# Optimization experiments

Measured on AMD Instinct MI355X. Metric: run time of the kernel, lower is better.

The kernel has to match this reference:

```python
import jax, jax.numpy as jnp
import numpy as np

B, T, C = 4, 2048, 1024
NH = 16
HD = C // NH


def setup_inputs() -> dict:
    key = jax.random.key(0)
    k1, k2, k3 = jax.random.split(key, 3)
    x = jax.random.normal(k1, (B, T, C), dtype=jnp.float32)
    Wqkv = jax.random.normal(k2, (C, 3 * C), dtype=jnp.float32) * 0.02
    bqkv = jnp.zeros((3 * C,), dtype=jnp.float32)
    Wproj = jax.random.normal(k3, (C, C), dtype=jnp.float32) * 0.02
    bproj = jnp.zeros((C,), dtype=jnp.float32)
    return {"x": x, "Wqkv": Wqkv, "bqkv": bqkv, "Wproj": Wproj, "bproj": bproj}


def reference(x, Wqkv, bqkv, Wproj, bproj):
    Bx, Tx, Cx = x.shape
    qkv = x @ Wqkv + bqkv  # [B,T,3C]
    q, k, v = jnp.split(qkv, 3, axis=-1)
    # [B, NH, T, HD]
    q = q.reshape(Bx, Tx, NH, HD).transpose(0, 2, 1, 3)
    k = k.reshape(Bx, Tx, NH, HD).transpose(0, 2, 1, 3)
    v = v.reshape(Bx, Tx, NH, HD).transpose(0, 2, 1, 3)
    scale = 1.0 / jnp.sqrt(jnp.float32(HD))
    att = jnp.einsum('bhqd,bhkd->bhqk', q, k) * scale  # [B,NH,T,T]
    causal = jnp.tril(jnp.ones((Tx, Tx), dtype=bool))
    att = jnp.where(causal, att, jnp.float32(-jnp.inf))
    att = jax.nn.softmax(att, axis=-1)
    y = jnp.einsum('bhqk,bhkd->bhqd', att, v)  # [B,NH,T,HD]
    y = y.transpose(0, 2, 1, 3).reshape(Bx, Tx, Cx)
    return y @ Wproj + bproj
```

## Files before the change

### kernel.cpp

```cpp
#include <hip/hip_runtime.h>
#include <hip/hip_bf16.h>
#include <math.h>

#define B_  4
#define T_  2048
#define C_  1024
#define NH_ 16
#define HD_ 64

using bf16 = __hip_bfloat16;
typedef __attribute__((ext_vector_type(8))) short bf16x8;
typedef __attribute__((ext_vector_type(4))) short bf16x4;
typedef __attribute__((ext_vector_type(4))) float f32x4;

__device__ __forceinline__ bf16 f2b(float f){ return __float2bfloat16(f); }

__device__ __forceinline__ short f2bs(float f){
  union { float f; unsigned u; } x; x.f = f;
  x.u += 0x7FFFu + ((x.u >> 16) & 1u);
  return (short)(x.u >> 16);
}

__device__ __forceinline__ bf16x4 pack_bf16x4(float a, float b, float c, float d){
  union { bf16x4 v; __hip_bfloat162 h[2]; } u;
  u.h[0] = __float22bfloat162_rn(make_float2(a, b));
  u.h[1] = __float22bfloat162_rn(make_float2(c, d));
  return u.v;
}

__device__ __forceinline__ float fexp2(float x){
  float r; asm("v_exp_f32 %0, %1" : "=v"(r) : "v"(x)); return r;
}

__device__ __forceinline__ void async_load16(const bf16* g, bf16* l){
  __builtin_amdgcn_global_load_lds((const __attribute__((address_space(1))) unsigned int*)g,
                                   (__attribute__((address_space(3))) unsigned int*)l,
                                   16, 0, 0);
}

#define QSCALE 0.18033688011112042f

__global__ __launch_bounds__(256) void k_prep(const float* __restrict__ x, bf16* __restrict__ xb, int n,
                                              const float* __restrict__ in0, bf16* __restrict__ out0,
                                              const float* __restrict__ in1, bf16* __restrict__ out1){
  __shared__ float t[32][33];
  int b = blockIdx.x;
  if (b < 8192){
    int i = (b * 256 + threadIdx.x) * 4;
    if (i < n){
      float4 f = *(const float4*)(x + i);
      ushort4 u;
      u.x = (unsigned short)f2bs(f.x);
      u.y = (unsigned short)f2bs(f.y);
      u.z = (unsigned short)f2bs(f.z);
      u.w = (unsigned short)f2bs(f.w);
      *(ushort4*)(xb + i) = u;
    }
    return;
  }
  b -= 8192;
  const float* in; bf16* out; int Cc, bx, by;
  if (b < 3072){ in = in0; out = out0; Cc = 3*C_; bx = (b % 96)*32; by = (b / 96)*32; }
  else { b -= 3072; in = in1; out = out1; Cc = C_; bx = (b & 31)*32; by = (b >> 5)*32; }
  const int R = C_;
  int lx = threadIdx.x & 31, ly = threadIdx.x >> 5;
  #pragma unroll
  for (int s = 0; s < 4; s++){
    int k = by + ly + s*8;
    t[ly + s*8][lx] = in[(size_t)k * Cc + bx + lx];
  }
  __syncthreads();
  #pragma unroll
  for (int s = 0; s < 4; s++){
    int n2 = bx + ly + s*8;
    out[(size_t)n2 * R + by + lx] = f2b(t[lx][ly + s*8]);
  }
}

template<int MODE, int BM>
__global__ __launch_bounds__(BM*2) void k_gemm(
    const bf16* __restrict__ A, const bf16* __restrict__ BT,
    const float* __restrict__ bias,
    bf16* __restrict__ qo, bf16* __restrict__ ko, bf16* __restrict__ vo,
    float* __restrict__ fout,
    int M, int N, int K)
{
  constexpr int NTHR = BM*2;
  constexpr int WMW  = BM/64;
  constexpr int NB   = 512/NTHR;
  __shared__ bf16 As[2][BM*32];
  __shared__ bf16 Bs[2][128*32];

  const int tid  = threadIdx.x;
  const int wave = tid >> 6, lane = tid & 63;
  const int wm = wave % WMW, wn = wave / WMW;
  const int quad = lane >> 4, l15 = lane & 15;
  const int bm = blockIdx.x * BM;
  const int bn = blockIdx.y * 128;

  const bf16* gA[2]; bf16* lA[2];
  #pragma unroll
  for (int s = 0; s < 2; s++){
    const int c = tid + s*NTHR;
    const int r = c >> 2, p = (c & 3) ^ ((r >> 1) & 3);
    gA[s] = A + (size_t)(bm + r)*K + p*8;
    lA[s] = &As[0][0] + (size_t)c*8;
  }
  const bf16* gB[NB]; bf16* lB[NB];
  #pragma unroll
  for (int s = 0; s < NB; s++){
    const int c = tid + s*NTHR;
    const int r = c >> 2, p = (c & 3) ^ ((r >> 1) & 3);
    gB[s] = BT + (size_t)(bn + r)*K + p*8;
    lB[s] = &Bs[0][0] + (size_t)c*8;
  }
  const int fsw = (l15 >> 1) & 3;

  f32x4 acc[4][4] = {};
  const int nK = K >> 5;

  #pragma unroll
  for (int s = 0; s < 2; s++) async_load16(gA[s], lA[s]);
  #pragma unroll
  for (int s = 0; s < NB; s++) async_load16(gB[s], lB[s]);

  for (int kt = 0; kt < nK; kt++){
    __syncthreads();
    if (kt + 1 < nK){
      const int off = (kt + 1) * 32;
      const int ba  = ((kt + 1) & 1) * (BM*32);
      const int bb  = ((kt + 1) & 1) * 4096;
      #pragma unroll
      for (int s = 0; s < 2; s++) async_load16(gA[s] + off, lA[s] + ba);
      #pragma unroll
      for (int s = 0; s < NB; s++) async_load16(gB[s] + off, lB[s] + bb);
    }
    const bf16* as = &As[kt & 1][0];
    const bf16* bs = &Bs[kt & 1][0];

    bf16x8 af[4], bfv[4];
    #pragma unroll
    for (int i = 0; i < 4; i++)
      af[i]  = *reinterpret_cast<const bf16x8*>(as + (wm*64 + i*16 + l15)*32 + ((quad ^ fsw) << 3));
    #pragma unroll
    for (int j = 0; j < 4; j++)
      bfv[j] = *reinterpret_cast<const bf16x8*>(bs + (wn*64 + j*16 + l15)*32 + ((quad ^ fsw) << 3));
    #pragma unroll
    for (int i = 0; i < 4; i++)
      #pragma unroll
      for (int j = 0; j < 4; j++)
        acc[i][j] = __builtin_amdgcn_mfma_f32_16x16x32_bf16(af[i], bfv[j], acc[i][j], 0, 0, 0);
  }

  if (MODE == 0){
    const int sec = bn >> 10;
    const int bb2 = bm >> 11;
    const int tb  = (bm & (T_ - 1)) + wm*64 + quad*4;
    const int hn  = ((bn & 1023) >> 6) + wn;
    const size_t bhx = (size_t)(bb2 * NH_ + hn);
    if (sec == 2){
      #pragma unroll
      for (int j = 0; j < 4; j++){
        const int d = j*16 + l15;
        const float bj = bias[bn + wn*64 + j*16 + l15];
        bf16* vrow = vo + (bhx * HD_ + d) * (size_t)T_;
        const int sw = (l15 & 7) * 8;
        #pragma unroll
        for (int i = 0; i < 4; i++){
          const int t = (tb + i*16) ^ sw;
          *reinterpret_cast<bf16x4*>(vrow + t) =
            pack_bf16x4(acc[i][j][0] + bj, acc[i][j][1] + bj,
                        acc[i][j][2] + bj, acc[i][j][3] + bj);
        }
      }
    } else {
      bf16* dst = (sec == 0) ? qo : ko;
      const float sc = (sec == 0) ? QSCALE : 1.0f;
      bf16* base = dst + bhx * T_ * HD_;
      float bj[4];
      #pragma unroll
      for (int j = 0; j < 4; j++) bj[j] = bias[bn + wn*64 + j*16 + l15];
      #pragma unroll
      for (int i = 0; i < 4; i++){
        #pragma unroll
        for (int r = 0; r < 4; r++){
          const int t  = tb + i*16 + r;
          const int sw2 = (t & 7) * 8;
          bf16* prow = base + (size_t)t * HD_;
          #pragma unroll
          for (int j = 0; j < 4; j++){
            const int dq = (j*16 + l15) ^ sw2;
            short s = f2bs((acc[i][j][r] + bj[j]) * sc);
            prow[dq] = *(bf16*)&s;
          }
        }
      }
    }
  } else {
    const int n0 = bn + wn*64 + l15;
    float bj[4];
    #pragma unroll
    for (int j = 0; j < 4; j++) bj[j] = bias[n0 + j*16];
    #pragma unroll
    for (int i = 0; i < 4; i++){
      #pragma unroll
      for (int r = 0; r < 4; r++){
        float* p0 = fout + (size_t)(bm + wm*64 + i*16 + quad*4 + r) * N + n0;
        #pragma unroll
        for (int j = 0; j < 4; j++)
          p0[j*16] = acc[i][j][r] + bj[j];
      }
    }
  }
}

__global__ __launch_bounds__(256) void k_attn(
    const bf16* __restrict__ Q, const bf16* __restrict__ Kg,
    const bf16* __restrict__ Vt, bf16* __restrict__ Y)
{
  __shared__ bf16 Ks[2][64*64];
  __shared__ bf16 Vs[2][64*64];

  const int bh = blockIdx.x;
  const int bb = bh >> 4, hh = bh & 15;
  const int qt = 15 - blockIdx.y;
  const int tid  = threadIdx.x;
  const int wave = tid >> 6, lane = tid & 63;
  const int quad = lane >> 4, l15 = lane & 15;
  const int swz  = (l15 & 7) * 8;

  const size_t baseQK = (size_t)bh * T_ * HD_;
  const size_t baseV  = (size_t)bh * HD_ * T_;

  const int ca = wave, cb = wave + 4;
  const bf16* kg_a = Kg + baseQK + ca*512 + (size_t)lane*8;
  const bf16* kg_b = Kg + baseQK + cb*512 + (size_t)lane*8;
  const bf16* vg_a = Vt + baseV + (size_t)(ca*8 + (lane>>3)) * T_ + (lane&7)*8;
  const bf16* vg_b = Vt + baseV + (size_t)(cb*8 + (lane>>3)) * T_ + (lane&7)*8;
  bf16* kl_a0 = &Ks[0][0] + ca*512;  bf16* kl_b0 = &Ks[0][0] + cb*512;
  bf16* vl_a0 = &Vs[0][0] + ca*512;  bf16* vl_b0 = &Vs[0][0] + cb*512;

  bf16x4 ones_f;
  {
    short v = (l15 == 0) ? f2bs(1.0f) : (short)0;
    ones_f = (bf16x4){ v, v, v, v };
  }

  const int jmax = 2*qt + 1;

  bf16x8 qf[2][2];
  #pragma unroll
  for (int s = 0; s < 2; s++){
    const int t = qt*128 + s*64 + wave*16 + l15;
    #pragma unroll
    for (int ks = 0; ks < 2; ks++){
      const int col = (ks*32 + quad*8) ^ swz;
      qf[s][ks] = *reinterpret_cast<const bf16x8*>(Q + baseQK + (size_t)t*HD_ + col);
    }
  }

  async_load16(kg_a, kl_a0);  async_load16(kg_b, kl_b0);
  async_load16(vg_a, vl_a0);  async_load16(vg_b, vl_b0);

  f32x4 o[2][5] = {};

  for (int j = 0; j <= jmax; j++){
    __syncthreads();

    if (j < jmax){
      const int nb = ((j+1) & 1) * 4096;
      const size_t ko = (size_t)(j+1) * 64 * HD_;
      async_load16(kg_a + ko, kl_a0 + nb);  async_load16(kg_b + ko, kl_b0 + nb);
      async_load16(vg_a + (j+1)*64, vl_a0 + nb);
      async_load16(vg_b + (j+1)*64, vl_b0 + nb);
    }

    const bf16* ksb = &Ks[j & 1][0];
    const bf16* vsb = &Vs[j & 1][0];

    f32x4 st[2][4] = {};
    __builtin_amdgcn_s_setprio(1);
    #pragma unroll
    for (int ks = 0; ks < 2; ks++){
      #pragma unroll
      for (int tk = 0; tk < 4; tk++){
        bf16x8 kf = *reinterpret_cast<const bf16x8*>(ksb + (tk*16 + l15)*64 + ((ks*32 + quad*8) ^ swz));
        st[0][tk] = __builtin_amdgcn_mfma_f32_16x16x32_bf16(kf, qf[0][ks], st[0][tk], 0, 0, 0);
        st[1][tk] = __builtin_amdgcn_mfma_f32_16x16x32_bf16(kf, qf[1][ks], st[1][tk], 0, 0, 0);
      }
    }
    __builtin_amdgcn_s_setprio(0);

    bf16x4 pf[2][4];
    #pragma unroll
    for (int s = 0; s < 2; s++){
      const int qg = qt*128 + s*64 + wave*16 + l15;
      const bool msk = s ? (j > 2*qt) : (j >= 2*qt);
      #pragma unroll
      for (int tk = 0; tk < 4; tk++){
        float e[4];
        #pragma unroll
        for (int r = 0; r < 4; r++){
          float sv = st[s][tk][r];
          if (msk){
            const int kvg = j*64 + tk*16 + quad*4 + r;
            if (kvg > qg) sv = -1e30f;
          }
          e[r] = fexp2(sv);
        }
        pf[s][tk] = pack_bf16x4(e[0], e[1], e[2], e[3]);
      }
    }

    __builtin_amdgcn_s_setprio(1);
    #pragma unroll
    for (int td = 0; td < 4; td++){
      #pragma unroll
      for (int tk = 0; tk < 4; tk++){
        bf16x4 vf = *reinterpret_cast<const bf16x4*>(vsb + (td*16 + l15)*64 + ((tk*16 + quad*4) ^ swz));
        o[0][td] = __builtin_amdgcn_mfma_f32_16x16x16bf16_1k(vf, pf[0][tk], o[0][td], 0, 0, 0);
        o[1][td] = __builtin_amdgcn_mfma_f32_16x16x16bf16_1k(vf, pf[1][tk], o[1][td], 0, 0, 0);
      }
    }
    #pragma unroll
    for (int tk = 0; tk < 4; tk++){
      o[0][4] = __builtin_amdgcn_mfma_f32_16x16x16bf16_1k(ones_f, pf[0][tk], o[0][4], 0, 0, 0);
      o[1][4] = __builtin_amdgcn_mfma_f32_16x16x16bf16_1k(ones_f, pf[1][tk], o[1][4], 0, 0, 0);
    }
    __builtin_amdgcn_s_setprio(0);
  }

  #pragma unroll
  for (int s = 0; s < 2; s++){
    const float l = __shfl(o[s][4][0], l15, 64);
    const float inv = 1.0f / l;
    const int t = qt*128 + s*64 + wave*16 + l15;
    bf16* yrow = Y + ((size_t)(bb * T_ + t)) * C_ + hh * HD_;
    #pragma unroll
    for (int td = 0; td < 4; td++){
      *reinterpret_cast<bf16x4*>(yrow + td*16 + quad*4) =
        pack_bf16x4(o[s][td][0] * inv, o[s][td][1] * inv,
                    o[s][td][2] * inv, o[s][td][3] * inv);
    }
  }
}


extern "C" void kernel_launch(void* const* d_in, const int* in_sizes, int n_in,
                              void* d_out, int out_size, void* d_ws, size_t ws_size,
                              hipStream_t stream) {
  const float* x     = (const float*)d_in[0];
  const float* Wqkv  = (const float*)d_in[1];
  const float* bqkv  = (const float*)d_in[2];
  const float* Wproj = (const float*)d_in[3];
  const float* bproj = (const float*)d_in[4];
  float* out = (float*)d_out;

  const size_t M = (size_t)B_ * T_;
  char* w = (char*)d_ws;
  bf16* xb     = (bf16*)w;  w += M * C_ * 2;
  bf16* WqkvT  = (bf16*)w;  w += (size_t)3 * C_ * C_ * 2;
  bf16* WprojT = (bf16*)w;  w += (size_t)C_ * C_ * 2;
  bf16* Qb     = (bf16*)w;  w += M * C_ * 2;
  bf16* Kb     = (bf16*)w;  w += M * C_ * 2;
  bf16* Vtb    = (bf16*)w;  w += M * C_ * 2;
  bf16* Yb     = (bf16*)w;  w += M * C_ * 2;

  {
    int n = (int)(M * C_);
    k_prep<<<dim3(12288), dim3(256), 0, stream>>>(x, xb, n, Wqkv, WqkvT, Wproj, WprojT);
  }
  k_gemm<0,256><<<dim3(M/256, (3*C_)/128), dim3(512), 0, stream>>>(
      xb, WqkvT, bqkv, Qb, Kb, Vtb, nullptr, (int)M, 3*C_, C_);
  k_attn<<<dim3(64, 16), dim3(256), 0, stream>>>(Qb, Kb, Vtb, Yb);
  k_gemm<1,128><<<dim3(M/128, C_/128), dim3(256), 0, stream>>>(
      Yb, WprojT, bproj, nullptr, nullptr, nullptr, out, (int)M, C_, C_);
}
```

Before: 247.0 us.

## Rework GEMM pipeline with 64-wide K stages and manual vmcnt waits

```diff
diff --git a/kernel.cpp b/kernel.cpp
--- a/kernel.cpp
+++ b/kernel.cpp
@@ -77,79 +77,82 @@
   }
 }
 
-template<int MODE, int BM>
-__global__ __launch_bounds__(BM*2) void k_gemm(
+template<int MODE>
+__global__ __launch_bounds__(256, 2) void k_gemm8(
     const bf16* __restrict__ A, const bf16* __restrict__ BT,
     const float* __restrict__ bias,
     bf16* __restrict__ qo, bf16* __restrict__ ko, bf16* __restrict__ vo,
     float* __restrict__ fout,
     int M, int N, int K)
 {
-  constexpr int NTHR = BM*2;
-  constexpr int WMW  = BM/64;
-  constexpr int NB   = 512/NTHR;
-  __shared__ bf16 As[2][BM*32];
-  __shared__ bf16 Bs[2][128*32];
+  __shared__ bf16 As[2][2][128*32];
+  __shared__ bf16 Bs[2][2][128*32];
 
   const int tid  = threadIdx.x;
   const int wave = tid >> 6, lane = tid & 63;
-  const int wm = wave % WMW, wn = wave / WMW;
+  const int wm = wave & 1, wn = wave >> 1;
   const int quad = lane >> 4, l15 = lane & 15;
-  const int bm = blockIdx.x * BM;
+  const int bm = blockIdx.x * 128;
   const int bn = blockIdx.y * 128;
 
-  const bf16* gA[2]; bf16* lA[2];
+  const bf16* gA[2]; const bf16* gB[2]; int lofs[2];
   #pragma unroll
   for (int s = 0; s < 2; s++){
-    const int c = tid + s*NTHR;
+    const int c = tid + s*256;
     const int r = c >> 2, p = (c & 3) ^ ((r >> 1) & 3);
-    gA[s] = A + (size_t)(bm + r)*K + p*8;
-    lA[s] = &As[0][0] + (size_t)c*8;
-  }
-  const bf16* gB[NB]; bf16* lB[NB];
-  #pragma unroll
-  for (int s = 0; s < NB; s++){
-    const int c = tid + s*NTHR;
-    const int r = c >> 2, p = (c & 3) ^ ((r >> 1) & 3);
+    gA[s] = A  + (size_t)(bm + r)*K + p*8;
     gB[s] = BT + (size_t)(bn + r)*K + p*8;
-    lB[s] = &Bs[0][0] + (size_t)c*8;
+    lofs[s] = c*8;
   }
   const int fsw = (l15 >> 1) & 3;
 
   f32x4 acc[4][4] = {};
-  const int nK = K >> 5;
-
-  #pragma unroll
-  for (int s = 0; s < 2; s++) async_load16(gA[s], lA[s]);
-  #pragma unroll
-  for (int s = 0; s < NB; s++) async_load16(gB[s], lB[s]);
-
-  for (int kt = 0; kt < nK; kt++){
-    __syncthreads();
-    if (kt + 1 < nK){
-      const int off = (kt + 1) * 32;
-      const int ba  = ((kt + 1) & 1) * (BM*32);
-      const int bb  = ((kt + 1) & 1) * 4096;
-      #pragma unroll
-      for (int s = 0; s < 2; s++) async_load16(gA[s] + off, lA[s] + ba);
-      #pragma unroll
-      for (int s = 0; s < NB; s++) async_load16(gB[s] + off, lB[s] + bb);
-    }
-    const bf16* as = &As[kt & 1][0];
-    const bf16* bs = &Bs[kt & 1][0];
-
-    bf16x8 af[4], bfv[4];
-    #pragma unroll
-    for (int i = 0; i < 4; i++)
-      af[i]  = *reinterpret_cast<const bf16x8*>(as + (wm*64 + i*16 + l15)*32 + ((quad ^ fsw) << 3));
-    #pragma unroll
-    for (int j = 0; j < 4; j++)
-      bfv[j] = *reinterpret_cast<const bf16x8*>(bs + (wn*64 + j*16 + l15)*32 + ((quad ^ fsw) << 3));
-    #pragma unroll
-    for (int i = 0; i < 4; i++)
+  const int nT = K >> 6;
+
+  #pragma unroll
+  for (int kh = 0; kh < 2; kh++)
+    #pragma unroll
+    for (int s = 0; s < 2; s++){
+      async_load16(gA[s] + kh*32, &As[0][kh][0] + lofs[s]);
+      async_load16(gB[s] + kh*32, &Bs[0][kh][0] + lofs[s]);
+    }
+
+  for (int u = 0; u < nT; u++){
+    const int d = u & 1;
+    #pragma unroll
+    for (int kh = 0; kh < 2; kh++){
+      if (u + 1 < nT || kh == 0) asm volatile("s_waitcnt vmcnt(4)" ::: "memory");
+      else                       asm volatile("s_waitcnt vmcnt(0)" ::: "memory");
+      __builtin_amdgcn_s_barrier();
+      __builtin_amdgcn_sched_barrier(0);
+
+      const bf16* as = &As[d][kh][0];
+      const bf16* bs = &Bs[d][kh][0];
+      bf16x8 af[4], bfv[4];
+      #pragma unroll
+      for (int i = 0; i < 4; i++)
+        af[i]  = *reinterpret_cast<const bf16x8*>(as + (wm*64 + i*16 + l15)*32 + ((quad ^ fsw) << 3));
       #pragma unroll
       for (int j = 0; j < 4; j++)
-        acc[i][j] = __builtin_amdgcn_mfma_f32_16x16x32_bf16(af[i], bfv[j], acc[i][j], 0, 0, 0);
+        bfv[j] = *reinterpret_cast<const bf16x8*>(bs + (wn*64 + j*16 + l15)*32 + ((quad ^ fsw) << 3));
+
+      if (u + 1 < nT){
+        const int ko2 = (u + 1)*64 + kh*32;
+        #pragma unroll
+        for (int s = 0; s < 2; s++){
+          async_load16(gA[s] + ko2, &As[d^1][kh][0] + lofs[s]);
+          async_load16(gB[s] + ko2, &Bs[d^1][kh][0] + lofs[s]);
+        }
+      }
+
+      __builtin_amdgcn_s_setprio(1);
+      #pragma unroll
+      for (int i = 0; i < 4; i++)
+        #pragma unroll
+        for (int j = 0; j < 4; j++)
+          acc[i][j] = __builtin_amdgcn_mfma_f32_16x16x32_bf16(af[i], bfv[j], acc[i][j], 0, 0, 0);
+      __builtin_amdgcn_s_setprio(0);
+    }
   }
 
   if (MODE == 0){
@@ -161,9 +164,9 @@
     if (sec == 2){
       #pragma unroll
       for (int j = 0; j < 4; j++){
-        const int d = j*16 + l15;
+        const int d2 = j*16 + l15;
         const float bj = bias[bn + wn*64 + j*16 + l15];
-        bf16* vrow = vo + (bhx * HD_ + d) * (size_t)T_;
+        bf16* vrow = vo + (bhx * HD_ + d2) * (size_t)T_;
         const int sw = (l15 & 7) * 8;
         #pragma unroll
         for (int i = 0; i < 4; i++){
@@ -245,6 +248,7 @@
     short v = (l15 == 0) ? f2bs(1.0f) : (short)0;
     ones_f = (bf16x4){ v, v, v, v };
   }
+  const f32x4 ZV = {0.0f, 0.0f, 0.0f, 0.0f};
 
   const int jmax = 2*qt + 1;
 
@@ -278,16 +282,16 @@
     const bf16* ksb = &Ks[j & 1][0];
     const bf16* vsb = &Vs[j & 1][0];
 
-    f32x4 st[2][4] = {};
+    f32x4 st[2][4];
     __builtin_amdgcn_s_setprio(1);
     #pragma unroll
-    for (int ks = 0; ks < 2; ks++){
-      #pragma unroll
-      for (int tk = 0; tk < 4; tk++){
-        bf16x8 kf = *reinterpret_cast<const bf16x8*>(ksb + (tk*16 + l15)*64 + ((ks*32 + quad*8) ^ swz));
-        st[0][tk] = __builtin_amdgcn_mfma_f32_16x16x32_bf16(kf, qf[0][ks], st[0][tk], 0, 0, 0);
-        st[1][tk] = __builtin_amdgcn_mfma_f32_16x16x32_bf16(kf, qf[1][ks], st[1][tk], 0, 0, 0);
-      }
+    for (int tk = 0; tk < 4; tk++){
+      bf16x8 kf0 = *reinterpret_cast<const bf16x8*>(ksb + (tk*16 + l15)*64 + ((quad*8) ^ swz));
+      bf16x8 kf1 = *reinterpret_cast<const bf16x8*>(ksb + (tk*16 + l15)*64 + ((32 + quad*8) ^ swz));
+      st[0][tk] = __builtin_amdgcn_mfma_f32_16x16x32_bf16(kf0, qf[0][0], ZV, 0, 0, 0);
+      st[1][tk] = __builtin_amdgcn_mfma_f32_16x16x32_bf16(kf0, qf[1][0], ZV, 0, 0, 0);
+      st[0][tk] = __builtin_amdgcn_mfma_f32_16x16x32_bf16(kf1, qf[0][1], st[0][tk], 0, 0, 0);
+      st[1][tk] = __builtin_amdgcn_mfma_f32_16x16x32_bf16(kf1, qf[1][1], st[1][tk], 0, 0, 0);
     }
     __builtin_amdgcn_s_setprio(0);
 
@@ -370,9 +374,9 @@
     int n = (int)(M * C_);
     k_prep<<<dim3(12288), dim3(256), 0, stream>>>(x, xb, n, Wqkv, WqkvT, Wproj, WprojT);
   }
-  k_gemm<0,256><<<dim3(M/256, (3*C_)/128), dim3(512), 0, stream>>>(
+  k_gemm8<0><<<dim3(M/128, (3*C_)/128), dim3(256), 0, stream>>>(
       xb, WqkvT, bqkv, Qb, Kb, Vtb, nullptr, (int)M, 3*C_, C_);
   k_attn<<<dim3(64, 16), dim3(256), 0, stream>>>(Qb, Kb, Vtb, Yb);
-  k_gemm<1,128><<<dim3(M/128, C_/128), dim3(256), 0, stream>>>(
+  k_gemm8<1><<<dim3(M/128, C_/128), dim3(256), 0, stream>>>(
       Yb, WprojT, bproj, nullptr, nullptr, nullptr, out, (int)M, C_, C_);
 }
```

After: 236.7 us. 1.04x faster.
